# Kernel optimization log

Measured on AMD Instinct MI355X. Metric: run time of the kernel, lower is better.

## Reference

```python
import jax, jax.numpy as jnp
import numpy as np

H = 128
IN = 2048
PROJ = 64
EPS = 1e-5


def setup_inputs() -> dict:
    key = jax.random.key(0)
    ks = jax.random.split(key, 12)
    B, T = 64, 512
    s_in = 1.0 / np.sqrt(H)  # torch RNN init: U(-1/sqrt(H), 1/sqrt(H))
    u = lambda k, shape, s: jax.random.uniform(k, shape, jnp.float32, -s, s)
    return {
        "x": jax.random.normal(ks[0], (B, T, IN), jnp.float32),
        "W_ih1": u(ks[1], (H, IN), s_in),
        "W_hh1": u(ks[2], (H, H), s_in),
        "b_ih1": u(ks[3], (H,), s_in),
        "b_hh1": u(ks[4], (H,), s_in),
        "W_ih2": u(ks[5], (H, H), s_in),
        "W_hh2": u(ks[6], (H, H), s_in),
        "b_ih2": u(ks[7], (H,), s_in),
        "b_hh2": u(ks[8], (H,), s_in),
        "W_proj": u(ks[9], (PROJ, H), 1.0 / np.sqrt(H)),
        "b_proj": u(ks[10], (PROJ,), 1.0 / np.sqrt(H)),
        "gamma": jnp.ones((PROJ,), jnp.float32),
        "beta": jnp.zeros((PROJ,), jnp.float32),
    }


def _rnn(xproj, W_hh, collect):
    # xproj: [B, T, H] = x @ W_ih^T + b_ih + b_hh (biases folded in)
    B = xproj.shape[0]
    h0 = jnp.zeros((B, H), xproj.dtype)
    xs = jnp.swapaxes(xproj, 0, 1)  # [T, B, H]

    def step(h, xp):
        h = jnp.tanh(xp + h @ W_hh.T)
        return h, (h if collect else None)

    h_last, ys = jax.lax.scan(step, h0, xs)
    return h_last, (jnp.swapaxes(ys, 0, 1) if collect else None)


def reference(x, W_ih1, W_hh1, b_ih1, b_hh1, W_ih2, W_hh2, b_ih2, b_hh2,
              W_proj, b_proj, gamma, beta):
    # layer 1: hoist the big input GEMM out of the recurrence
    xp1 = jnp.einsum("bti,hi->bth", x, W_ih1) + (b_ih1 + b_hh1)
    _, y1 = _rnn(xp1, W_hh1, collect=True)  # [B, T, H]
    # layer 2: only final hidden state is needed
    xp2 = jnp.einsum("bth,gh->btg", y1, W_ih2) + (b_ih2 + b_hh2)
    h2, _ = _rnn(xp2, W_hh2, collect=False)  # [B, H]
    # projection + LayerNorm
    z = h2 @ W_proj.T + b_proj  # [B, 64]
    mu = jnp.mean(z, axis=-1, keepdims=True)
    var = jnp.mean((z - mu) ** 2, axis=-1, keepdims=True)
    return (z - mu) * jax.lax.rsqrt(var + EPS) * gamma + beta
```

## Files before the change

### kernel.cpp

```cpp
#include <hip/hip_runtime.h>
#include <math.h>

#define H 128
#define IN 2048
#define PROJ 64
#define BT 32768
#define T_STEPS 512
#define BATCH 64
#define BM 128
#define BKA 64

using f32x4  = __attribute__((ext_vector_type(4))) float;
using bfrag  = __attribute__((ext_vector_type(8))) short;
using h2_t   = __attribute__((ext_vector_type(2))) _Float16;

__device__ __forceinline__ unsigned cvtpk(float lo, float hi) {
  unsigned r;
  asm("v_cvt_pk_bf16_f32 %0, %1, %2" : "=v"(r) : "v"(lo), "v"(hi));
  return r;
}

__global__ __launch_bounds__(512) void xp1_gemm(
    const float* __restrict__ x, const float* __restrict__ W,
    const float* __restrict__ b1, const float* __restrict__ b2,
    float* __restrict__ xp1) {
  __shared__ __align__(16) char As[2][BM * BKA * 2];
  __shared__ __align__(16) char Bs[2][H * BKA * 2];
  const int t  = threadIdx.x;
  const int m0 = blockIdx.x * BM;
  const int wv = t >> 6, l = t & 63;
  const int wm = wv >> 2;
  const int wn = wv & 3;
  const int lr = l & 15;
  const int lq = l >> 4;

  const float* xg[4];
  const float* wg[4];
  int so[4];
#pragma unroll
  for (int i = 0; i < 4; ++i) {
    int c = t + 512 * i, r = c >> 4, k4 = c & 15;
    xg[i] = x + (size_t)(m0 + r) * IN + k4 * 4;
    wg[i] = W + (size_t)r * IN + k4 * 4;
    so[i] = (r * 128 + k4 * 8) ^ ((r & 7) << 4);
  }
  int ao[2][4], bo[2][2];
#pragma unroll
  for (int kf = 0; kf < 2; ++kf) {
#pragma unroll
    for (int mf = 0; mf < 4; ++mf) {
      int r = wm * 64 + mf * 16 + lr;
      ao[kf][mf] = (r * 128 + kf * 64 + lq * 16) ^ ((r & 7) << 4);
    }
#pragma unroll
    for (int nf = 0; nf < 2; ++nf) {
      int r = wn * 32 + nf * 16 + lr;
      bo[kf][nf] = (r * 128 + kf * 64 + lq * 16) ^ ((r & 7) << 4);
    }
  }

  f32x4 acc[4][2];
#pragma unroll
  for (int mf = 0; mf < 4; ++mf)
#pragma unroll
    for (int nf = 0; nf < 2; ++nf)
#pragma unroll
      for (int j = 0; j < 4; ++j) acc[mf][nf][j] = 0.f;

  float4 xr[4], wr[4];
#pragma unroll
  for (int i = 0; i < 4; ++i) {
    xr[i] = *(const float4*)&xg[i][0];
    wr[i] = *(const float4*)&wg[i][0];
  }
#pragma unroll
  for (int i = 0; i < 4; ++i) {
    uint2 ux; ux.x = cvtpk(xr[i].x, xr[i].y); ux.y = cvtpk(xr[i].z, xr[i].w);
    *(uint2*)(As[0] + so[i]) = ux;
    uint2 uw; uw.x = cvtpk(wr[i].x, wr[i].y); uw.y = cvtpk(wr[i].z, wr[i].w);
    *(uint2*)(Bs[0] + so[i]) = uw;
  }
  __syncthreads();

  for (int tc = 0; tc < 32; ++tc) {
    const int kc = (tc + 1) * BKA;
    if (tc < 31) {
#pragma unroll
      for (int i = 0; i < 4; ++i) {
        xr[i] = *(const float4*)&xg[i][kc];
        wr[i] = *(const float4*)&wg[i][kc];
      }
    }
    const char* Ab = As[tc & 1];
    const char* Bb = Bs[tc & 1];
#pragma unroll
    for (int kf = 0; kf < 2; ++kf) {
      bfrag af[4], bf[2];
#pragma unroll
      for (int mf = 0; mf < 4; ++mf) af[mf] = *(const bfrag*)(Ab + ao[kf][mf]);
#pragma unroll
      for (int nf = 0; nf < 2; ++nf) bf[nf] = *(const bfrag*)(Bb + bo[kf][nf]);
#pragma unroll
      for (int mf = 0; mf < 4; ++mf)
#pragma unroll
        for (int nf = 0; nf < 2; ++nf)
          acc[mf][nf] = __builtin_amdgcn_mfma_f32_16x16x32_bf16(
              af[mf], bf[nf], acc[mf][nf], 0, 0, 0);
    }
    if (tc < 31) {
      char* Aw = As[(tc + 1) & 1];
      char* Bw = Bs[(tc + 1) & 1];
#pragma unroll
      for (int i = 0; i < 4; ++i) {
        uint2 ux; ux.x = cvtpk(xr[i].x, xr[i].y); ux.y = cvtpk(xr[i].z, xr[i].w);
        *(uint2*)(Aw + so[i]) = ux;
        uint2 uw; uw.x = cvtpk(wr[i].x, wr[i].y); uw.y = cvtpk(wr[i].z, wr[i].w);
        *(uint2*)(Bw + so[i]) = uw;
      }
    }
    __syncthreads();
  }

#pragma unroll
  for (int nf = 0; nf < 2; ++nf) {
    int n = wn * 32 + nf * 16 + lr;
    float bias = b1[n] + b2[n];
#pragma unroll
    for (int mf = 0; mf < 4; ++mf) {
      int mr = m0 + wm * 64 + mf * 16 + lq * 4;
#pragma unroll
      for (int j = 0; j < 4; ++j)
        xp1[(size_t)(mr + j) * H + n] = acc[mf][nf][j] + bias;
    }
  }
}

struct Wrow { unsigned p0, p1, p2, p3, p4, p5, p6, p7; };

__device__ __forceinline__ unsigned pkh(float x, float y) {
  h2_t p = {(_Float16)x, (_Float16)y};
  return __builtin_bit_cast(unsigned, p);
}

__device__ __forceinline__ float d2(unsigned w, int h, float acc) {
  return __builtin_amdgcn_fdot2(__builtin_bit_cast(h2_t, w),
                                __builtin_bit_cast(h2_t, (unsigned)h), acc,
                                false);
}

__device__ __forceinline__ float dot16(Wrow w, int4 lo, int4 hi, float acc) {
  acc = d2(w.p0, lo.x, acc);
  acc = d2(w.p1, lo.y, acc);
  acc = d2(w.p2, lo.z, acc);
  acc = d2(w.p3, lo.w, acc);
  acc = d2(w.p4, hi.x, acc);
  acc = d2(w.p5, hi.y, acc);
  acc = d2(w.p6, hi.z, acc);
  acc = d2(w.p7, hi.w, acc);
  return acc;
}

__device__ __forceinline__ Wrow loadrow(const float* p) {
  float4 a = *(const float4*)p;
  float4 b = *(const float4*)(p + 4);
  float4 c = *(const float4*)(p + 8);
  float4 d = *(const float4*)(p + 12);
  Wrow w = {pkh(a.x, a.y), pkh(a.z, a.w), pkh(b.x, b.y), pkh(b.z, b.w),
            pkh(c.x, c.y), pkh(c.z, c.w), pkh(d.x, d.y), pkh(d.z, d.w)};
  return w;
}

#define PIN(W)                                                              \
  asm volatile("" : "+v"(W.p0), "+v"(W.p1), "+v"(W.p2), "+v"(W.p3),         \
                    "+v"(W.p4), "+v"(W.p5), "+v"(W.p6), "+v"(W.p7))

template <int CTRL>
__device__ __forceinline__ float dpp_add(float x) {
  return x + __builtin_bit_cast(
                 float, __builtin_amdgcn_mov_dpp(__builtin_bit_cast(int, x),
                                                 CTRL, 0xf, 0xf, true));
}

__device__ __forceinline__ float red8(float v) {
  v = dpp_add<0xB1>(v);
  v = dpp_add<0x4E>(v);
  v = dpp_add<0x141>(v);
  return v;
}

__device__ __forceinline__ float fast_tanh(float x) {
  float e = __expf(2.0f * x);
  return 1.0f - 2.0f / (e + 1.0f);
}

__global__ __launch_bounds__(512)
__attribute__((amdgpu_waves_per_eu(1, 2)))
void rnn_fused(
    const float* __restrict__ xp1,
    const float* __restrict__ W_hh1, const float* __restrict__ W_ih2,
    const float* __restrict__ W_hh2, const float* __restrict__ b_ih2,
    const float* __restrict__ b_hh2, const float* __restrict__ W_proj,
    const float* __restrict__ b_proj, const float* __restrict__ gamma,
    const float* __restrict__ beta, float* __restrict__ out) {
  __shared__ __align__(16) _Float16 h1s[2][H];
  __shared__ __align__(16) _Float16 h2s[2][H];
  const int t = threadIdx.x;
  const int b = blockIdx.x;
  const int l = t & 63;
  const int w = t >> 6;
  const int g = (l >> 3) & 7;
  const int q = l & 7;
  const int r0 = 16 * w + g;
  const int r1 = r0 + 8;

  Wrow W1r0 = loadrow(&W_hh1[r0 * H + 16 * q]);
  Wrow W1r1 = loadrow(&W_hh1[r1 * H + 16 * q]);
  Wrow W2r0 = loadrow(&W_ih2[r0 * H + 16 * q]);
  Wrow W2r1 = loadrow(&W_ih2[r1 * H + 16 * q]);
  Wrow W3r0 = loadrow(&W_hh2[r0 * H + 16 * q]);
  Wrow W3r1 = loadrow(&W_hh2[r1 * H + 16 * q]);
  PIN(W1r0); PIN(W1r1); PIN(W2r0); PIN(W2r1); PIN(W3r0); PIN(W3r1);

  const float bias2_0 = b_ih2[r0] + b_hh2[r0];
  const float bias2_1 = b_ih2[r1] + b_hh2[r1];

  if (t < H) { h1s[0][t] = (_Float16)0.f; h2s[0][t] = (_Float16)0.f; }
  __syncthreads();

  const float* xpr0 = xp1 + (size_t)b * T_STEPS * H + r0;
  const float* xpr1 = xpr0 + 8;
  float xpA0 = xpr0[0];
  float xpA1 = xpr1[0];

  for (int ts = 0; ts < T_STEPS; ++ts) {
    PIN(W1r0); PIN(W1r1); PIN(W2r0); PIN(W2r1); PIN(W3r0); PIN(W3r1);

    const int cur = ts & 1;
    const _Float16* h1p = h1s[cur];
    const _Float16* h2p = h2s[cur];
    _Float16* h1w = h1s[cur ^ 1];
    _Float16* h2w = h2s[cur ^ 1];

    float nx0 = 0.f, nx1 = 0.f;
    if (ts + 1 < T_STEPS) {
      nx0 = xpr0[(size_t)(ts + 1) * H];
      nx1 = xpr1[(size_t)(ts + 1) * H];
    }

    int4 l1 = *(const int4*)&h1p[16 * q];
    int4 u1 = *(const int4*)&h1p[16 * q + 8];
    int4 l2 = *(const int4*)&h2p[16 * q];
    int4 u2 = *(const int4*)&h2p[16 * q + 8];
    float a0 = dot16(W1r0, l1, u1, 0.f);
    float a1 = dot16(W1r1, l1, u1, 0.f);
    float c0 = dot16(W3r0, l2, u2, 0.f);
    float c1 = dot16(W3r1, l2, u2, 0.f);
    a0 = red8(a0); a1 = red8(a1);
    c0 = red8(c0); c1 = red8(c1);
    float h1n0 = fast_tanh(xpA0 + a0);
    float h1n1 = fast_tanh(xpA1 + a1);
    if (q == 0) { h1w[r0] = (_Float16)h1n0; h1w[r1] = (_Float16)h1n1; }
    __syncthreads();

    int4 nl = *(const int4*)&h1w[16 * q];
    int4 nu = *(const int4*)&h1w[16 * q + 8];
    float bb0 = dot16(W2r0, nl, nu, 0.f);
    float bb1 = dot16(W2r1, nl, nu, 0.f);
    bb0 = red8(bb0); bb1 = red8(bb1);
    float h2n0 = fast_tanh(bias2_0 + bb0 + c0);
    float h2n1 = fast_tanh(bias2_1 + bb1 + c1);
    if (q == 0) { h2w[r0] = (_Float16)h2n0; h2w[r1] = (_Float16)h2n1; }
    __syncthreads();
    xpA0 = nx0; xpA1 = nx1;
  }

  if (t < PROJ) {
    const float* wp = W_proj + t * H;
    float z = b_proj[t];
#pragma unroll
    for (int i = 0; i < 32; ++i) {
      float4 wv = *(const float4*)&wp[4 * i];
      z = fmaf(wv.x, (float)h2s[0][4 * i + 0], z);
      z = fmaf(wv.y, (float)h2s[0][4 * i + 1], z);
      z = fmaf(wv.z, (float)h2s[0][4 * i + 2], z);
      z = fmaf(wv.w, (float)h2s[0][4 * i + 3], z);
    }
    float s = z;
#pragma unroll
    for (int d = 1; d < 64; d <<= 1) s += __shfl_xor(s, d);
    float mu = s * 0.015625f;
    float dz = z - mu;
    float v = dz * dz;
#pragma unroll
    for (int d = 1; d < 64; d <<= 1) v += __shfl_xor(v, d);
    float rstd = rsqrtf(v * 0.015625f + 1e-5f);
    out[b * PROJ + t] = dz * rstd * gamma[t] + beta[t];
  }
}

extern "C" void kernel_launch(void* const* d_in, const int* in_sizes, int n_in,
                              void* d_out, int out_size, void* d_ws, size_t ws_size,
                              hipStream_t stream) {
  const float* x      = (const float*)d_in[0];
  const float* W_ih1  = (const float*)d_in[1];
  const float* W_hh1  = (const float*)d_in[2];
  const float* b_ih1  = (const float*)d_in[3];
  const float* b_hh1  = (const float*)d_in[4];
  const float* W_ih2  = (const float*)d_in[5];
  const float* W_hh2  = (const float*)d_in[6];
  const float* b_ih2  = (const float*)d_in[7];
  const float* b_hh2  = (const float*)d_in[8];
  const float* W_proj = (const float*)d_in[9];
  const float* b_proj = (const float*)d_in[10];
  const float* gamma  = (const float*)d_in[11];
  const float* beta   = (const float*)d_in[12];

  float* xp1 = (float*)d_ws;

  xp1_gemm<<<BT / BM, 512, 0, stream>>>(x, W_ih1, b_ih1, b_hh1, xp1);
  rnn_fused<<<BATCH, 512, 0, stream>>>(xp1, W_hh1, W_ih2, W_hh2, b_ih2, b_hh2,
                                       W_proj, b_proj, gamma, beta,
                                       (float*)d_out);
}
```

Before: 486.9 us.

## Batch 16 sequences per block and run recurrence with MFMA, skewing layers

The recurrence kernel now processes 16 batch rows per block and computes the per-step matvecs as 16x16x32 f16 MFMA matrix products, with weights held as B fragments in registers. Layer 2 is skewed one step behind layer 1, so both layers share one barrier per step instead of two. Hidden states go to swizzled LDS tiles. This swaps a latency-bound dot2/DPP chain over 64 blocks for fewer, denser blocks (4 total), which lowers GPU parallelism and risks longer per-step latency.

```diff
diff --git a/kernel.cpp b/kernel.cpp
--- a/kernel.cpp
+++ b/kernel.cpp
@@ -9,10 +9,12 @@
 #define BATCH 64
 #define BM 128
 #define BKA 64
+#define BTILE 16
+#define NBLK (BATCH / BTILE)
 
 using f32x4  = __attribute__((ext_vector_type(4))) float;
 using bfrag  = __attribute__((ext_vector_type(8))) short;
-using h2_t   = __attribute__((ext_vector_type(2))) _Float16;
+using f16x8v = __attribute__((ext_vector_type(8))) _Float16;
 
 __device__ __forceinline__ unsigned cvtpk(float lo, float hi) {
   unsigned r;
@@ -135,62 +137,26 @@
   }
 }
 
-struct Wrow { unsigned p0, p1, p2, p3, p4, p5, p6, p7; };
-
-__device__ __forceinline__ unsigned pkh(float x, float y) {
-  h2_t p = {(_Float16)x, (_Float16)y};
-  return __builtin_bit_cast(unsigned, p);
-}
-
-__device__ __forceinline__ float d2(unsigned w, int h, float acc) {
-  return __builtin_amdgcn_fdot2(__builtin_bit_cast(h2_t, w),
-                                __builtin_bit_cast(h2_t, (unsigned)h), acc,
-                                false);
-}
-
-__device__ __forceinline__ float dot16(Wrow w, int4 lo, int4 hi, float acc) {
-  acc = d2(w.p0, lo.x, acc);
-  acc = d2(w.p1, lo.y, acc);
-  acc = d2(w.p2, lo.z, acc);
-  acc = d2(w.p3, lo.w, acc);
-  acc = d2(w.p4, hi.x, acc);
-  acc = d2(w.p5, hi.y, acc);
-  acc = d2(w.p6, hi.z, acc);
-  acc = d2(w.p7, hi.w, acc);
-  return acc;
-}
-
-__device__ __forceinline__ Wrow loadrow(const float* p) {
-  float4 a = *(const float4*)p;
-  float4 b = *(const float4*)(p + 4);
-  float4 c = *(const float4*)(p + 8);
-  float4 d = *(const float4*)(p + 12);
-  Wrow w = {pkh(a.x, a.y), pkh(a.z, a.w), pkh(b.x, b.y), pkh(b.z, b.w),
-            pkh(c.x, c.y), pkh(c.z, c.w), pkh(d.x, d.y), pkh(d.z, d.w)};
-  return w;
-}
-
-#define PIN(W)                                                              \
-  asm volatile("" : "+v"(W.p0), "+v"(W.p1), "+v"(W.p2), "+v"(W.p3),         \
-                    "+v"(W.p4), "+v"(W.p5), "+v"(W.p6), "+v"(W.p7))
-
-template <int CTRL>
-__device__ __forceinline__ float dpp_add(float x) {
-  return x + __builtin_bit_cast(
-                 float, __builtin_amdgcn_mov_dpp(__builtin_bit_cast(int, x),
-                                                 CTRL, 0xf, 0xf, true));
-}
-
-__device__ __forceinline__ float red8(float v) {
-  v = dpp_add<0xB1>(v);
-  v = dpp_add<0x4E>(v);
-  v = dpp_add<0x141>(v);
-  return v;
+
+__device__ __forceinline__ void bar() {
+  asm volatile("s_waitcnt lgkmcnt(0)\n\ts_barrier" ::: "memory");
 }
 
 __device__ __forceinline__ float fast_tanh(float x) {
   float e = __expf(2.0f * x);
   return 1.0f - 2.0f / (e + 1.0f);
+}
+
+__device__ __forceinline__ void wh(char* base, int b, int n, float v) {
+  *(_Float16*)(base + ((b * 256 + n * 2) ^ ((b & 7) << 4))) = (_Float16)v;
+}
+
+__device__ __forceinline__ f16x8v ldfrag(const float* Wm, int n, int k) {
+  float4 lo = *(const float4*)&Wm[n * H + k];
+  float4 hi = *(const float4*)&Wm[n * H + k + 4];
+  f16x8v r = {(_Float16)lo.x, (_Float16)lo.y, (_Float16)lo.z, (_Float16)lo.w,
+              (_Float16)hi.x, (_Float16)hi.y, (_Float16)hi.z, (_Float16)hi.w};
+  return r;
 }
 
 __global__ __launch_bounds__(512)
@@ -202,99 +168,147 @@
     const float* __restrict__ b_hh2, const float* __restrict__ W_proj,
     const float* __restrict__ b_proj, const float* __restrict__ gamma,
     const float* __restrict__ beta, float* __restrict__ out) {
-  __shared__ __align__(16) _Float16 h1s[2][H];
-  __shared__ __align__(16) _Float16 h2s[2][H];
-  const int t = threadIdx.x;
-  const int b = blockIdx.x;
-  const int l = t & 63;
-  const int w = t >> 6;
-  const int g = (l >> 3) & 7;
-  const int q = l & 7;
-  const int r0 = 16 * w + g;
-  const int r1 = r0 + 8;
-
-  Wrow W1r0 = loadrow(&W_hh1[r0 * H + 16 * q]);
-  Wrow W1r1 = loadrow(&W_hh1[r1 * H + 16 * q]);
-  Wrow W2r0 = loadrow(&W_ih2[r0 * H + 16 * q]);
-  Wrow W2r1 = loadrow(&W_ih2[r1 * H + 16 * q]);
-  Wrow W3r0 = loadrow(&W_hh2[r0 * H + 16 * q]);
-  Wrow W3r1 = loadrow(&W_hh2[r1 * H + 16 * q]);
-  PIN(W1r0); PIN(W1r1); PIN(W2r0); PIN(W2r1); PIN(W3r0); PIN(W3r1);
-
-  const float bias2_0 = b_ih2[r0] + b_hh2[r0];
-  const float bias2_1 = b_ih2[r1] + b_hh2[r1];
-
-  if (t < H) { h1s[0][t] = (_Float16)0.f; h2s[0][t] = (_Float16)0.f; }
-  __syncthreads();
-
-  const float* xpr0 = xp1 + (size_t)b * T_STEPS * H + r0;
-  const float* xpr1 = xpr0 + 8;
-  float xpA0 = xpr0[0];
-  float xpA1 = xpr1[0];
-
-  for (int ts = 0; ts < T_STEPS; ++ts) {
-    PIN(W1r0); PIN(W1r1); PIN(W2r0); PIN(W2r1); PIN(W3r0); PIN(W3r1);
-
-    const int cur = ts & 1;
-    const _Float16* h1p = h1s[cur];
-    const _Float16* h2p = h2s[cur];
-    _Float16* h1w = h1s[cur ^ 1];
-    _Float16* h2w = h2s[cur ^ 1];
-
-    float nx0 = 0.f, nx1 = 0.f;
-    if (ts + 1 < T_STEPS) {
-      nx0 = xpr0[(size_t)(ts + 1) * H];
-      nx1 = xpr1[(size_t)(ts + 1) * H];
-    }
-
-    int4 l1 = *(const int4*)&h1p[16 * q];
-    int4 u1 = *(const int4*)&h1p[16 * q + 8];
-    int4 l2 = *(const int4*)&h2p[16 * q];
-    int4 u2 = *(const int4*)&h2p[16 * q + 8];
-    float a0 = dot16(W1r0, l1, u1, 0.f);
-    float a1 = dot16(W1r1, l1, u1, 0.f);
-    float c0 = dot16(W3r0, l2, u2, 0.f);
-    float c1 = dot16(W3r1, l2, u2, 0.f);
-    a0 = red8(a0); a1 = red8(a1);
-    c0 = red8(c0); c1 = red8(c1);
-    float h1n0 = fast_tanh(xpA0 + a0);
-    float h1n1 = fast_tanh(xpA1 + a1);
-    if (q == 0) { h1w[r0] = (_Float16)h1n0; h1w[r1] = (_Float16)h1n1; }
-    __syncthreads();
-
-    int4 nl = *(const int4*)&h1w[16 * q];
-    int4 nu = *(const int4*)&h1w[16 * q + 8];
-    float bb0 = dot16(W2r0, nl, nu, 0.f);
-    float bb1 = dot16(W2r1, nl, nu, 0.f);
-    bb0 = red8(bb0); bb1 = red8(bb1);
-    float h2n0 = fast_tanh(bias2_0 + bb0 + c0);
-    float h2n1 = fast_tanh(bias2_1 + bb1 + c1);
-    if (q == 0) { h2w[r0] = (_Float16)h2n0; h2w[r1] = (_Float16)h2n1; }
-    __syncthreads();
-    xpA0 = nx0; xpA1 = nx1;
-  }
-
-  if (t < PROJ) {
-    const float* wp = W_proj + t * H;
-    float z = b_proj[t];
-#pragma unroll
-    for (int i = 0; i < 32; ++i) {
-      float4 wv = *(const float4*)&wp[4 * i];
-      z = fmaf(wv.x, (float)h2s[0][4 * i + 0], z);
-      z = fmaf(wv.y, (float)h2s[0][4 * i + 1], z);
-      z = fmaf(wv.z, (float)h2s[0][4 * i + 2], z);
-      z = fmaf(wv.w, (float)h2s[0][4 * i + 3], z);
-    }
-    float s = z;
-#pragma unroll
-    for (int d = 1; d < 64; d <<= 1) s += __shfl_xor(s, d);
+  __shared__ __align__(16) char h1s[2][BTILE * H * 2];
+  __shared__ __align__(16) char h2s[2][BTILE * H * 2];
+  const int t  = threadIdx.x;
+  const int l  = t & 63;
+  const int nw = t >> 6;
+  const int n0 = nw * 16;
+  const int lc = l & 15;
+  const int lk = l >> 4;
+  const int bq = blockIdx.x * BTILE;
+
+  const int n = n0 + lc;
+  f16x8v B1[4], B2[4], B3[4];
+#pragma unroll
+  for (int ks = 0; ks < 4; ++ks) {
+    const int k = ks * 32 + lk * 8;
+    B1[ks] = ldfrag(W_hh1, n, k);
+    B2[ks] = ldfrag(W_ih2, n, k);
+    B3[ks] = ldfrag(W_hh2, n, k);
+  }
+  const float bias2 = b_ih2[n] + b_hh2[n];
+
+  const int rb = lk * 4;
+  const float* xq0 = xp1 + ((size_t)(bq + rb + 0) * T_STEPS) * H + n;
+  const float* xq1 = xp1 + ((size_t)(bq + rb + 1) * T_STEPS) * H + n;
+  const float* xq2 = xp1 + ((size_t)(bq + rb + 2) * T_STEPS) * H + n;
+  const float* xq3 = xp1 + ((size_t)(bq + rb + 3) * T_STEPS) * H + n;
+
+  *(float2*)&h1s[1][8 * t] = float2{0.f, 0.f};
+  *(float2*)&h2s[1][8 * t] = float2{0.f, 0.f};
+
+  {
+    float x0 = xq0[0], x1 = xq1[0], x2 = xq2[0], x3 = xq3[0];
+    wh(h1s[0], rb + 0, n, fast_tanh(x0));
+    wh(h1s[0], rb + 1, n, fast_tanh(x1));
+    wh(h1s[0], rb + 2, n, fast_tanh(x2));
+    wh(h1s[0], rb + 3, n, fast_tanh(x3));
+  }
+  bar();
+
+  float xpc0 = xq0[H], xpc1 = xq1[H], xpc2 = xq2[H], xpc3 = xq3[H];
+
+#pragma unroll 1
+  for (int i = 1; i < T_STEPS; ++i) {
+    const char* h1p = h1s[(i - 1) & 1];
+    const char* h2p = h2s[i & 1];
+    char* h1w = h1s[i & 1];
+    char* h2w = h2s[(i - 1) & 1];
+
+    float nx0 = 0.f, nx1 = 0.f, nx2 = 0.f, nx3 = 0.f;
+    if (i + 1 < T_STEPS) {
+      size_t o = (size_t)(i + 1) * H;
+      nx0 = xq0[o]; nx1 = xq1[o]; nx2 = xq2[o]; nx3 = xq3[o];
+    }
+
+    f16x8v a1[4], a2[4];
+#pragma unroll
+    for (int ks = 0; ks < 4; ++ks) {
+      const int off = (lc * 256 + ks * 64 + lk * 16) ^ ((lc & 7) << 4);
+      a1[ks] = *(const f16x8v*)(h1p + off);
+      a2[ks] = *(const f16x8v*)(h2p + off);
+    }
+
+    f32x4 acc1 = {xpc0, xpc1, xpc2, xpc3};
+    f32x4 acc2 = {bias2, bias2, bias2, bias2};
+    f32x4 acc3 = {0.f, 0.f, 0.f, 0.f};
+#pragma unroll
+    for (int ks = 0; ks < 4; ++ks) {
+      acc1 = __builtin_amdgcn_mfma_f32_16x16x32_f16(a1[ks], B1[ks], acc1, 0, 0, 0);
+      acc2 = __builtin_amdgcn_mfma_f32_16x16x32_f16(a1[ks], B2[ks], acc2, 0, 0, 0);
+      acc3 = __builtin_amdgcn_mfma_f32_16x16x32_f16(a2[ks], B3[ks], acc3, 0, 0, 0);
+    }
+
+    wh(h1w, rb + 0, n, fast_tanh(acc1[0]));
+    wh(h1w, rb + 1, n, fast_tanh(acc1[1]));
+    wh(h1w, rb + 2, n, fast_tanh(acc1[2]));
+    wh(h1w, rb + 3, n, fast_tanh(acc1[3]));
+    wh(h2w, rb + 0, n, fast_tanh(acc2[0] + acc3[0]));
+    wh(h2w, rb + 1, n, fast_tanh(acc2[1] + acc3[1]));
+    wh(h2w, rb + 2, n, fast_tanh(acc2[2] + acc3[2]));
+    wh(h2w, rb + 3, n, fast_tanh(acc2[3] + acc3[3]));
+    bar();
+    xpc0 = nx0; xpc1 = nx1; xpc2 = nx2; xpc3 = nx3;
+  }
+
+  {
+    const char* h1p = h1s[1];
+    const char* h2p = h2s[0];
+    char* h2w = h2s[1];
+    f16x8v a1[4], a2[4];
+#pragma unroll
+    for (int ks = 0; ks < 4; ++ks) {
+      const int off = (lc * 256 + ks * 64 + lk * 16) ^ ((lc & 7) << 4);
+      a1[ks] = *(const f16x8v*)(h1p + off);
+      a2[ks] = *(const f16x8v*)(h2p + off);
+    }
+    f32x4 acc2 = {bias2, bias2, bias2, bias2};
+    f32x4 acc3 = {0.f, 0.f, 0.f, 0.f};
+#pragma unroll
+    for (int ks = 0; ks < 4; ++ks) {
+      acc2 = __builtin_amdgcn_mfma_f32_16x16x32_f16(a1[ks], B2[ks], acc2, 0, 0, 0);
+      acc3 = __builtin_amdgcn_mfma_f32_16x16x32_f16(a2[ks], B3[ks], acc3, 0, 0, 0);
+    }
+    wh(h2w, rb + 0, n, fast_tanh(acc2[0] + acc3[0]));
+    wh(h2w, rb + 1, n, fast_tanh(acc2[1] + acc3[1]));
+    wh(h2w, rb + 2, n, fast_tanh(acc2[2] + acc3[2]));
+    wh(h2w, rb + 3, n, fast_tanh(acc2[3] + acc3[3]));
+    bar();
+  }
+
+  {
+    const int bl = t >> 5;
+    const int pp = t & 31;
+    const char* hf = h2s[1];
+    float z0 = b_proj[pp], z1 = b_proj[pp + 32];
+#pragma unroll
+    for (int kc = 0; kc < 16; ++kc) {
+      f16x8v hv = *(const f16x8v*)(hf + ((bl * 256 + kc * 16) ^ ((bl & 7) << 4)));
+      float4 wa0 = *(const float4*)&W_proj[pp * H + kc * 8];
+      float4 wb0 = *(const float4*)&W_proj[pp * H + kc * 8 + 4];
+      float4 wa1 = *(const float4*)&W_proj[(pp + 32) * H + kc * 8];
+      float4 wb1 = *(const float4*)&W_proj[(pp + 32) * H + kc * 8 + 4];
+      z0 = fmaf(wa0.x, (float)hv[0], z0); z0 = fmaf(wa0.y, (float)hv[1], z0);
+      z0 = fmaf(wa0.z, (float)hv[2], z0); z0 = fmaf(wa0.w, (float)hv[3], z0);
+      z0 = fmaf(wb0.x, (float)hv[4], z0); z0 = fmaf(wb0.y, (float)hv[5], z0);
+      z0 = fmaf(wb0.z, (float)hv[6], z0); z0 = fmaf(wb0.w, (float)hv[7], z0);
+      z1 = fmaf(wa1.x, (float)hv[0], z1); z1 = fmaf(wa1.y, (float)hv[1], z1);
+      z1 = fmaf(wa1.z, (float)hv[2], z1); z1 = fmaf(wa1.w, (float)hv[3], z1);
+      z1 = fmaf(wb1.x, (float)hv[4], z1); z1 = fmaf(wb1.y, (float)hv[5], z1);
+      z1 = fmaf(wb1.z, (float)hv[6], z1); z1 = fmaf(wb1.w, (float)hv[7], z1);
+    }
+    float s = z0 + z1;
+#pragma unroll
+    for (int d = 1; d < 32; d <<= 1) s += __shfl_xor(s, d);
     float mu = s * 0.015625f;
-    float dz = z - mu;
-    float v = dz * dz;
-#pragma unroll
-    for (int d = 1; d < 64; d <<= 1) v += __shfl_xor(v, d);
+    float d0 = z0 - mu, d1 = z1 - mu;
+    float v = d0 * d0 + d1 * d1;
+#pragma unroll
+    for (int d = 1; d < 32; d <<= 1) v += __shfl_xor(v, d);
     float rstd = rsqrtf(v * 0.015625f + 1e-5f);
-    out[b * PROJ + t] = dz * rstd * gamma[t] + beta[t];
+    out[(bq + bl) * PROJ + pp]      = d0 * rstd * gamma[pp] + beta[pp];
+    out[(bq + bl) * PROJ + pp + 32] = d1 * rstd * gamma[pp + 32] + beta[pp + 32];
   }
 }
 
@@ -318,7 +332,7 @@
   float* xp1 = (float*)d_ws;
 
   xp1_gemm<<<BT / BM, 512, 0, stream>>>(x, W_ih1, b_ih1, b_hh1, xp1);
-  rnn_fused<<<BATCH, 512, 0, stream>>>(xp1, W_hh1, W_ih2, W_hh2, b_ih2, b_hh2,
-                                       W_proj, b_proj, gamma, beta,
-                                       (float*)d_out);
-}
+  rnn_fused<<<NBLK, 512, 0, stream>>>(xp1, W_hh1, W_ih2, W_hh2, b_ih2, b_hh2,
+                                      W_proj, b_proj, gamma, beta,
+                                      (float*)d_out);
+}
```

Measured after the change: 665.8 us. 1.37x slower.
